# Performance work log

Measured on AMD Instinct MI355X. Metric: run time of the kernel, lower is better.

## Reference

```python
import jax, jax.numpy as jnp
import numpy as np


def setup_inputs() -> dict:
    key = jax.random.key(0)
    ks = jax.random.split(key, 16)
    B, S, D, H = 32, 2048, 512, 512
    s = 1.0 / np.sqrt(H)
    inp = {
        "x": jax.random.normal(ks[0], (B, H), jnp.float32),
        "context": jax.random.normal(ks[1], (B, S, D), jnp.float32),
        "mask": jnp.zeros((B, S), jnp.bool_),  # False = valid position
        "Wi": jax.random.normal(ks[2], (H, H), jnp.float32) * s,
        "bi": jax.random.normal(ks[3], (H,), jnp.float32) * s,
        "Wc0": jax.random.normal(ks[4], (H, D), jnp.float32) * s,
        "bc0": jax.random.normal(ks[5], (H,), jnp.float32) * s,
        "Wc1": jax.random.normal(ks[6], (H, D), jnp.float32) * s,
        "bc1": jax.random.normal(ks[7], (H,), jnp.float32) * s,
        "Wc2": jax.random.normal(ks[8], (H, D), jnp.float32) * s,
        "bc2": jax.random.normal(ks[9], (H,), jnp.float32) * s,
        "Wc3": jax.random.normal(ks[10], (H, D), jnp.float32) * s,
        "bc3": jax.random.normal(ks[11], (H,), jnp.float32) * s,
        "V": jax.random.uniform(ks[12], (H,), jnp.float32, -s, s),
    }
    return inp


def reference(x, context, mask, Wi, bi, Wc0, bc0, Wc1, bc1, Wc2, bc2, Wc3, bc3, V):
    # mask: True = masked out in the original API; module flips it first.
    valid = ~mask  # [B, S], True = keep

    inp = (x @ Wi.T + bi)[:, :, None]  # [B, H, 1]

    def proj(W, b):
        # Conv1d(D, H, kernel=1) on context.permute(0,2,1) == token-wise GEMM
        return jnp.einsum("bsd,hd->bhs", context, W) + b[None, :, None]  # [B, H, S]

    ctx = jnp.concatenate(
        [proj(Wc0, bc0), proj(Wc1, bc1), proj(Wc2, bc2), proj(Wc3, bc3)], axis=2
    )  # [B, H, 4S]

    t = jnp.tanh(inp + ctx)                      # [B, H, 4S]
    att = jnp.einsum("h,bhs->bs", V, t)          # bmm(V[B,1,H], t).squeeze(1)
    att = 10.0 * jnp.tanh(att)                   # [B, 4S]

    valid4 = jnp.tile(valid, (1, 4))             # mask.repeat(1, 4)
    att = jnp.where(valid4, att, -jnp.inf)
    # torch.no_grad() around the masked fill detaches the rest of the graph
    att = jax.lax.stop_gradient(att)

    ans = jax.nn.softmax(att, axis=1)            # [B, 4S]
    p = jnp.max(ans, axis=1)
    indices = jnp.argmax(ans, axis=1)
    return indices[:, None], p[:, None], mask
```

## Files before the change

kernel.cpp:

```cpp
#include <hip/hip_runtime.h>
#include <math.h>

typedef __bf16 bf16x8 __attribute__((ext_vector_type(8)));
typedef float f32x4 __attribute__((ext_vector_type(4)));
typedef short short8v __attribute__((ext_vector_type(8)));

#define MARGIN 0.01f
#define NCAND 32

__device__ __forceinline__ unsigned short f2bf(float f) {
  unsigned u = __float_as_uint(f);
  u += 0x7fffu + ((u >> 16) & 1u);
  return (unsigned short)(u >> 16);
}
__device__ __forceinline__ float tanh_fast(float x) {
  float e = __builtin_amdgcn_exp2f(x * 2.885390081777927f);
  return 1.f - 2.f * __builtin_amdgcn_rcpf(e + 1.f);
}
__device__ __forceinline__ void gl_lds16(const void* g, void* l) {
  __builtin_amdgcn_global_load_lds(
      (const __attribute__((address_space(1))) unsigned int*)g,
      (__attribute__((address_space(3))) unsigned int*)l, 16, 0, 0);
}

__global__ __launch_bounds__(256) void prep_inp_k(const float* __restrict__ x,
    const float* __restrict__ Wi, const float* __restrict__ bi, float* __restrict__ inp) {
  int gid = blockIdx.x * 256 + threadIdx.x;
  int b = gid >> 9, h = gid & 511;
  const float* xr = x + b * 512;
  const float* wr = Wi + h * 512;
  float acc = bi[h];
  #pragma unroll 4
  for (int k = 0; k < 512; k += 4) {
    float4 xv = *(const float4*)(xr + k);
    float4 wv = *(const float4*)(wr + k);
    acc += xv.x * wv.x + xv.y * wv.y + xv.z * wv.z + xv.w * wv.w;
  }
  inp[gid] = acc;
}

__global__ __launch_bounds__(256) void prep_w_pack_k(const float* __restrict__ w0,
    const float* __restrict__ w1, const float* __restrict__ w2, const float* __restrict__ w3,
    short* __restrict__ Whi) {
  int gid = blockIdx.x * 256 + threadIdx.x;
  if (gid >= 131072) return;
  int c = gid & 3, row = (gid >> 2) & 255, TK = gid >> 10;
  int TN = TK >> 4, KS = TK & 15;
  int n = TN * 256 + row;
  int g = n >> 9, h = n & 511;
  const float* w = (g == 0) ? w0 : (g == 1) ? w1 : (g == 2) ? w2 : w3;
  int csrc = c ^ ((row >> 1) & 3);
  const float* src = w + (size_t)h * 512 + KS * 32 + csrc * 8;
  float f[8];
  *(float4*)&f[0] = *(const float4*)(src);
  *(float4*)&f[4] = *(const float4*)(src + 4);
  short8v hv;
  #pragma unroll
  for (int i = 0; i < 8; ++i) hv[i] = (short)f2bf(f[i]);
  *(short8v*)(Whi + (size_t)gid * 8) = hv;
}

__global__ __launch_bounds__(256) void prep_ctx_pack_k(const float* __restrict__ ctx,
    short* __restrict__ Chi) {
  int gid = blockIdx.x * 256 + threadIdx.x;
  int c = gid & 3, row = (gid >> 2) & 255, TK = gid >> 10;
  int TM = TK >> 4, KS = TK & 15;
  size_t m = (size_t)TM * 256 + row;
  int csrc = c ^ ((row >> 1) & 3);
  int k = KS * 32 + csrc * 8;
  float f[8];
  *(float4*)&f[0] = *(const float4*)(ctx + m * 512 + k);
  *(float4*)&f[4] = *(const float4*)(ctx + m * 512 + k + 4);
  short8v hv;
  #pragma unroll
  for (int i = 0; i < 8; ++i) hv[i] = (short)f2bf(f[i]);
  *(short8v*)(Chi + (size_t)gid * 8) = hv;
}

template<bool PRESPLIT>
__global__ __launch_bounds__(512, 2) void gemm_att_k(
    const float* __restrict__ ctx, const short* __restrict__ Chi,
    const short* __restrict__ Whi,
    const float* __restrict__ inp,
    const float* __restrict__ bc0, const float* __restrict__ bc1,
    const float* __restrict__ bc2, const float* __restrict__ bc3,
    const float* __restrict__ V, float* __restrict__ att) {
  __shared__ __align__(16) short smem[2][2][8192];
  __shared__ float sV[256], sPre[256];

  const int t = threadIdx.x;
  int d = blockIdx.x + (blockIdx.y << 3);
  int work = (d & 7) * 256 + (d >> 3);
  int mt = work >> 3, nt = work & 7;
  int b = mt >> 3;
  int g = nt >> 1, h0 = (nt & 1) * 256;

  if (t < 256) {
    const float* bc = (g == 0) ? bc0 : (g == 1) ? bc1 : (g == 2) ? bc2 : bc3;
    sV[t] = V[h0 + t];
    sPre[t] = inp[b * 512 + h0 + t] + bc[h0 + t];
  }

  const int toff = t * 8;
  auto stage = [&](int buf, int ks) {
    short* lb = &smem[buf][0][0];
    if (PRESPLIT) {
      const short* gA = Chi + (((size_t)mt * 16 + ks) << 13) + toff;
      gl_lds16(gA,        lb + toff);
      gl_lds16(gA + 4096, lb + toff + 4096);
    } else {
      int row = t >> 1, half = t & 1;
      const float* src = ctx + ((size_t)mt * 256 + row) * 512 + ks * 32 + half * 16;
      float f0[8], f1[8];
      *(float4*)&f0[0] = *(const float4*)(src);
      *(float4*)&f0[4] = *(const float4*)(src + 4);
      *(float4*)&f1[0] = *(const float4*)(src + 8);
      *(float4*)&f1[4] = *(const float4*)(src + 12);
      short8v h0v, h1v;
      #pragma unroll
      for (int i = 0; i < 8; ++i) { h0v[i] = (short)f2bf(f0[i]); h1v[i] = (short)f2bf(f1[i]); }
      int s = (row >> 1) & 3;
      int p0 = (half * 2) ^ s, p1 = (half * 2 + 1) ^ s;
      *(short8v*)&smem[buf][0][row * 32 + p0 * 8] = h0v;
      *(short8v*)&smem[buf][0][row * 32 + p1 * 8] = h1v;
    }
    const short* gB = Whi + (((size_t)nt * 16 + ks) << 13) + toff;
    gl_lds16(gB,        lb + 8192 + toff);
    gl_lds16(gB + 4096, lb + 8192 + toff + 4096);
  };

  f32x4 acc[8][4];
  #pragma unroll
  for (int i = 0; i < 8; ++i)
    #pragma unroll
    for (int j = 0; j < 4; ++j) acc[i][j] = (f32x4){0.f, 0.f, 0.f, 0.f};

  const int lane = t & 63, wid = t >> 6;
  const int wr = wid >> 2, wc = wid & 3;
  const int fr = lane & 15, fq = lane >> 4;
  const int csw = fq ^ ((fr >> 1) & 3);

  stage(0, 0);
  __syncthreads();

  for (int ks = 0; ks < 16; ++ks) {
    int cur = ks & 1;
    if (ks + 1 < 16) stage(cur ^ 1, ks + 1);

    const short* sa = &smem[cur][0][0];
    bf16x8 ah[8], bh[4];
    #pragma unroll
    for (int mi = 0; mi < 8; ++mi)
      ah[mi] = *(const bf16x8*)(sa + (wr * 128 + mi * 16 + fr) * 32 + csw * 8);
    #pragma unroll
    for (int ni = 0; ni < 4; ++ni)
      bh[ni] = *(const bf16x8*)(sa + 8192 + (wc * 64 + ni * 16 + fr) * 32 + csw * 8);
    #pragma unroll
    for (int mi = 0; mi < 8; ++mi)
      #pragma unroll
      for (int ni = 0; ni < 4; ++ni)
        acc[mi][ni] = __builtin_amdgcn_mfma_f32_16x16x32_bf16(ah[mi], bh[ni], acc[mi][ni], 0, 0, 0);
    __syncthreads();
  }

  float vV[4], vP[4];
  #pragma unroll
  for (int ni = 0; ni < 4; ++ni) {
    int j = wc * 64 + ni * 16 + fr;
    vV[ni] = sV[j];
    vP[ni] = sPre[j];
  }
  size_t abase = (size_t)b * 8192 + (size_t)g * 2048;
  #pragma unroll
  for (int mi = 0; mi < 8; ++mi) {
    #pragma unroll
    for (int r = 0; r < 4; ++r) {
      float sum = 0.f;
      #pragma unroll
      for (int ni = 0; ni < 4; ++ni)
        sum += vV[ni] * tanh_fast(vP[ni] + acc[mi][ni][r]);
      sum += __shfl_xor(sum, 1, 64);
      sum += __shfl_xor(sum, 2, 64);
      sum += __shfl_xor(sum, 4, 64);
      sum += __shfl_xor(sum, 8, 64);
      if (fr == 0) {
        int s = (mt * 256 + wr * 128 + mi * 16 + fq * 4 + r) & 2047;
        atomicAdd(&att[abase + s], sum);
      }
    }
  }
}

__global__ __launch_bounds__(256) void tail_k(const float* __restrict__ att,
    const unsigned char* __restrict__ mask, const float* __restrict__ ctx,
    const float* __restrict__ Wc0, const float* __restrict__ Wc1,
    const float* __restrict__ Wc2, const float* __restrict__ Wc3,
    const float* __restrict__ bc0, const float* __restrict__ bc1,
    const float* __restrict__ bc2, const float* __restrict__ bc3,
    const float* __restrict__ inp, const float* __restrict__ V,
    float* __restrict__ out) {
  int b = blockIdx.x, t = threadIdx.x;
  __shared__ float sred[256];
  __shared__ float sctx[512];
  __shared__ int scnt;
  __shared__ int scand_j[NCAND];
  __shared__ float scand_a[NCAND];
  __shared__ float sexact[NCAND];

  if (t == 0) scnt = 0;
  float bm = -1e30f;
  for (int j = t; j < 8192; j += 256) {
    if (mask[b * 2048 + (j & 2047)]) continue;
    bm = fmaxf(bm, att[(size_t)b * 8192 + j]);
  }
  sred[t] = bm;
  __syncthreads();
  for (int s2 = 128; s2 > 0; s2 >>= 1) {
    if (t < s2) sred[t] = fmaxf(sred[t], sred[t + s2]);
    __syncthreads();
  }
  float mx = sred[0];
  float Lref = 10.f * tanhf(mx);
  __syncthreads();
  float se = 0.f;
  for (int j = t; j < 8192; j += 256) {
    if (mask[b * 2048 + (j & 2047)]) continue;
    float a = att[(size_t)b * 8192 + j];
    se += expf(10.f * tanhf(a) - Lref);
    if (a >= mx - MARGIN) {
      int slot = atomicAdd(&scnt, 1);
      if (slot < NCAND) { scand_j[slot] = j; scand_a[slot] = a; }
    }
  }
  sred[t] = se;
  __syncthreads();
  for (int s2 = 128; s2 > 0; s2 >>= 1) {
    if (t < s2) sred[t] += sred[t + s2];
    __syncthreads();
  }
  float den = sred[0];
  int n = min(scnt, NCAND);
  for (int j = t; j < 2048; j += 256)
    out[64 + b * 2048 + j] = mask[b * 2048 + j] ? 1.0f : 0.0f;
  for (int i = 0; i < n; ++i) {
    int jj = scand_j[i];
    int g = jj >> 11, s = jj & 2047;
    const float* W  = (g == 0) ? Wc0 : (g == 1) ? Wc1 : (g == 2) ? Wc2 : Wc3;
    const float* bc = (g == 0) ? bc0 : (g == 1) ? bc1 : (g == 2) ? bc2 : bc3;
    const float* cr = ctx + ((size_t)b * 2048 + s) * 512;
    __syncthreads();
    sctx[t] = cr[t];
    sctx[t + 256] = cr[t + 256];
    __syncthreads();
    float total = 0.f;
    #pragma unroll
    for (int hh = 0; hh < 2; ++hh) {
      int h = t + hh * 256;
      const float* wr = W + (size_t)h * 512;
      float acc = 0.f;
      #pragma unroll 4
      for (int k = 0; k < 512; k += 4) {
        float4 wv = *(const float4*)(wr + k);
        acc += wv.x * sctx[k] + wv.y * sctx[k + 1] + wv.z * sctx[k + 2] + wv.w * sctx[k + 3];
      }
      total += V[h] * tanhf(inp[b * 512 + h] + bc[h] + acc);
    }
    sred[t] = total;
    __syncthreads();
    for (int s2 = 128; s2 > 0; s2 >>= 1) {
      if (t < s2) sred[t] += sred[t + s2];
      __syncthreads();
    }
    if (t == 0) sexact[i] = sred[0];
  }
  __syncthreads();
  if (t == 0) {
    float d = den, best = -1e30f;
    int bj = 0x7fffffff;
    for (int i = 0; i < n; ++i) {
      float e = sexact[i];
      int j = scand_j[i];
      d += expf(10.f * tanhf(e) - Lref) - expf(10.f * tanhf(scand_a[i]) - Lref);
      if (e > best || (e == best && j < bj)) { best = e; bj = j; }
    }
    out[b] = (float)bj;
    out[32 + b] = expf(10.f * tanhf(best) - Lref) / d;
  }
}

extern "C" void kernel_launch(void* const* d_in, const int* in_sizes, int n_in,
                              void* d_out, int out_size, void* d_ws, size_t ws_size,
                              hipStream_t stream) {
  const float* x    = (const float*)d_in[0];
  const float* ctx  = (const float*)d_in[1];
  const unsigned char* mask = (const unsigned char*)d_in[2];
  const float* Wi   = (const float*)d_in[3];
  const float* bi   = (const float*)d_in[4];
  const float* Wc0  = (const float*)d_in[5];
  const float* bc0  = (const float*)d_in[6];
  const float* Wc1  = (const float*)d_in[7];
  const float* bc1  = (const float*)d_in[8];
  const float* Wc2  = (const float*)d_in[9];
  const float* bc2  = (const float*)d_in[10];
  const float* Wc3  = (const float*)d_in[11];
  const float* bc3  = (const float*)d_in[12];
  const float* V    = (const float*)d_in[13];
  float* out = (float*)d_out;

  float* inp    = (float*)d_ws;
  float* att    = inp + 16384;
  short* Whi    = (short*)(att + 262144);
  short* Chi    = Whi + 1048576;
  size_t need = (size_t)((char*)(Chi + 33554432) - (char*)d_ws);
  bool presplit = ws_size >= need;

  hipMemsetAsync(att, 0, 262144 * sizeof(float), stream);
  prep_inp_k<<<64, 256, 0, stream>>>(x, Wi, bi, inp);
  prep_w_pack_k<<<512, 256, 0, stream>>>(Wc0, Wc1, Wc2, Wc3, Whi);
  if (presplit) {
    prep_ctx_pack_k<<<16384, 256, 0, stream>>>(ctx, Chi);
    gemm_att_k<true><<<dim3(8, 256), 512, 0, stream>>>(ctx, Chi, Whi,
        inp, bc0, bc1, bc2, bc3, V, att);
  } else {
    gemm_att_k<false><<<dim3(8, 256), 512, 0, stream>>>(ctx, nullptr, Whi,
        inp, bc0, bc1, bc2, bc3, V, att);
  }
  tail_k<<<32, 256, 0, stream>>>(att, mask, ctx, Wc0, Wc1, Wc2, Wc3,
      bc0, bc1, bc2, bc3, inp, V, out);
}
```

Before: 320.8 us.

## Use 64-wide K tiles with split-phase MFMA/load interleaving in GEMM

Doubles the K-tile from 32 to 64 so the main loop runs 8 iterations instead of 16. The packed bf16 layout and its XOR swizzle are changed to match. Each tile is split into four MFMA phases, with the A and B prefetches staggered between them. Explicit waitcnt, sched_barrier, s_barrier and setprio control the overlap of loads and matrix math. The aim is fewer barriers per K and better hiding of global-to-LDS latency, at the cost of twice the LDS footprint, which may limit the 2-blocks-per-CU occupancy.

Result: no change. 325.2 us (+1.4%).

```diff
diff --git a/kernel.cpp b/kernel.cpp
--- a/kernel.cpp
+++ b/kernel.cpp
@@ -7,6 +7,22 @@
 
 #define MARGIN 0.01f
 #define NCAND 32
+
+#define WAITL do { asm volatile("s_waitcnt lgkmcnt(0)" ::: "memory"); __builtin_amdgcn_sched_barrier(0); } while (0)
+#define WAITV do { asm volatile("s_waitcnt vmcnt(0)" ::: "memory"); __builtin_amdgcn_sched_barrier(0); } while (0)
+#define RBAR  do { __builtin_amdgcn_sched_barrier(0); __builtin_amdgcn_s_barrier(); } while (0)
+#define BARR  __builtin_amdgcn_s_barrier()
+
+#define MFMA_PHASE(NH, B0, B1) do { \
+    WAITL; \
+    __builtin_amdgcn_s_setprio(1); \
+    _Pragma("unroll") \
+    for (int mi = 0; mi < 8; ++mi) { \
+      acc[mi][2*(NH)]   = __builtin_amdgcn_mfma_f32_16x16x32_bf16(a[mi], (B0), acc[mi][2*(NH)],   0, 0, 0); \
+      acc[mi][2*(NH)+1] = __builtin_amdgcn_mfma_f32_16x16x32_bf16(a[mi], (B1), acc[mi][2*(NH)+1], 0, 0, 0); \
+    } \
+    __builtin_amdgcn_s_setprio(0); \
+  } while (0)
 
 __device__ __forceinline__ unsigned short f2bf(float f) {
   unsigned u = __float_as_uint(f);
@@ -44,16 +60,14 @@
     short* __restrict__ Whi) {
   int gid = blockIdx.x * 256 + threadIdx.x;
   if (gid >= 131072) return;
-  int c = gid & 3, row = (gid >> 2) & 255, TK = gid >> 10;
-  int TN = TK >> 4, KS = TK & 15;
-  int n = TN * 256 + row;
+  int s = gid & 7, r = (gid >> 3) & 255, KT = (gid >> 11) & 7, TN = gid >> 14;
+  int n = TN * 256 + r;
   int g = n >> 9, h = n & 511;
   const float* w = (g == 0) ? w0 : (g == 1) ? w1 : (g == 2) ? w2 : w3;
-  int csrc = c ^ ((row >> 1) & 3);
-  const float* src = w + (size_t)h * 512 + KS * 32 + csrc * 8;
+  int k = KT * 64 + ((s ^ (r & 7)) * 8);
   float f[8];
-  *(float4*)&f[0] = *(const float4*)(src);
-  *(float4*)&f[4] = *(const float4*)(src + 4);
+  *(float4*)&f[0] = *(const float4*)(w + (size_t)h * 512 + k);
+  *(float4*)&f[4] = *(const float4*)(w + (size_t)h * 512 + k + 4);
   short8v hv;
   #pragma unroll
   for (int i = 0; i < 8; ++i) hv[i] = (short)f2bf(f[i]);
@@ -63,11 +77,9 @@
 __global__ __launch_bounds__(256) void prep_ctx_pack_k(const float* __restrict__ ctx,
     short* __restrict__ Chi) {
   int gid = blockIdx.x * 256 + threadIdx.x;
-  int c = gid & 3, row = (gid >> 2) & 255, TK = gid >> 10;
-  int TM = TK >> 4, KS = TK & 15;
-  size_t m = (size_t)TM * 256 + row;
-  int csrc = c ^ ((row >> 1) & 3);
-  int k = KS * 32 + csrc * 8;
+  int s = gid & 7, r = (gid >> 3) & 255, KT = (gid >> 11) & 7, TM = gid >> 14;
+  size_t m = (size_t)TM * 256 + r;
+  int k = KT * 64 + ((s ^ (r & 7)) * 8);
   float f[8];
   *(float4*)&f[0] = *(const float4*)(ctx + m * 512 + k);
   *(float4*)&f[4] = *(const float4*)(ctx + m * 512 + k + 4);
@@ -85,7 +97,7 @@
     const float* __restrict__ bc0, const float* __restrict__ bc1,
     const float* __restrict__ bc2, const float* __restrict__ bc3,
     const float* __restrict__ V, float* __restrict__ att) {
-  __shared__ __align__(16) short smem[2][2][8192];
+  __shared__ __align__(16) short smem[2][2][16384];
   __shared__ float sV[256], sPre[256];
 
   const int t = threadIdx.x;
@@ -102,31 +114,37 @@
   }
 
   const int toff = t * 8;
-  auto stage = [&](int buf, int ks) {
-    short* lb = &smem[buf][0][0];
-    if (PRESPLIT) {
-      const short* gA = Chi + (((size_t)mt * 16 + ks) << 13) + toff;
-      gl_lds16(gA,        lb + toff);
-      gl_lds16(gA + 4096, lb + toff + 4096);
-    } else {
-      int row = t >> 1, half = t & 1;
-      const float* src = ctx + ((size_t)mt * 256 + row) * 512 + ks * 32 + half * 16;
-      float f0[8], f1[8];
-      *(float4*)&f0[0] = *(const float4*)(src);
-      *(float4*)&f0[4] = *(const float4*)(src + 4);
-      *(float4*)&f1[0] = *(const float4*)(src + 8);
-      *(float4*)&f1[4] = *(const float4*)(src + 12);
-      short8v h0v, h1v;
+  auto stageA = [&](int tile) {
+    const short* gA = Chi + ((size_t)(mt * 8 + tile)) * 16384 + toff;
+    short* lA = &smem[tile & 1][0][0];
+    gl_lds16(gA,         lA + toff);
+    gl_lds16(gA + 4096,  lA + toff + 4096);
+    gl_lds16(gA + 8192,  lA + toff + 8192);
+    gl_lds16(gA + 12288, lA + toff + 12288);
+  };
+  auto stageB = [&](int tile) {
+    const short* gB = Whi + ((size_t)(nt * 8 + tile)) * 16384 + toff;
+    short* lB = &smem[tile & 1][1][0];
+    gl_lds16(gB,         lB + toff);
+    gl_lds16(gB + 4096,  lB + toff + 4096);
+    gl_lds16(gB + 8192,  lB + toff + 8192);
+    gl_lds16(gB + 12288, lB + toff + 12288);
+  };
+  auto stageA_reg = [&](int tile) {
+    #pragma unroll
+    for (int pass = 0; pass < 4; ++pass) {
+      int cc = pass * 512 + t;
+      int s = cc & 7, r = cc >> 3;
+      int k = tile * 64 + ((s ^ (r & 7)) * 8);
+      const float* src = ctx + ((size_t)mt * 256 + r) * 512 + k;
+      float f[8];
+      *(float4*)&f[0] = *(const float4*)src;
+      *(float4*)&f[4] = *(const float4*)(src + 4);
+      short8v hv;
       #pragma unroll
-      for (int i = 0; i < 8; ++i) { h0v[i] = (short)f2bf(f0[i]); h1v[i] = (short)f2bf(f1[i]); }
-      int s = (row >> 1) & 3;
-      int p0 = (half * 2) ^ s, p1 = (half * 2 + 1) ^ s;
-      *(short8v*)&smem[buf][0][row * 32 + p0 * 8] = h0v;
-      *(short8v*)&smem[buf][0][row * 32 + p1 * 8] = h1v;
-    }
-    const short* gB = Whi + (((size_t)nt * 16 + ks) << 13) + toff;
-    gl_lds16(gB,        lb + 8192 + toff);
-    gl_lds16(gB + 4096, lb + 8192 + toff + 4096);
+      for (int i = 0; i < 8; ++i) hv[i] = (short)f2bf(f[i]);
+      *(short8v*)(&smem[tile & 1][0][r * 64 + s * 8]) = hv;
+    }
   };
 
   f32x4 acc[8][4];
@@ -138,29 +156,48 @@
   const int lane = t & 63, wid = t >> 6;
   const int wr = wid >> 2, wc = wid & 3;
   const int fr = lane & 15, fq = lane >> 4;
-  const int csw = fq ^ ((fr >> 1) & 3);
-
-  stage(0, 0);
-  __syncthreads();
-
-  for (int ks = 0; ks < 16; ++ks) {
-    int cur = ks & 1;
-    if (ks + 1 < 16) stage(cur ^ 1, ks + 1);
-
-    const short* sa = &smem[cur][0][0];
-    bf16x8 ah[8], bh[4];
-    #pragma unroll
-    for (int mi = 0; mi < 8; ++mi)
-      ah[mi] = *(const bf16x8*)(sa + (wr * 128 + mi * 16 + fr) * 32 + csw * 8);
-    #pragma unroll
-    for (int ni = 0; ni < 4; ++ni)
-      bh[ni] = *(const bf16x8*)(sa + 8192 + (wc * 64 + ni * 16 + fr) * 32 + csw * 8);
-    #pragma unroll
-    for (int mi = 0; mi < 8; ++mi)
-      #pragma unroll
-      for (int ni = 0; ni < 4; ++ni)
-        acc[mi][ni] = __builtin_amdgcn_mfma_f32_16x16x32_bf16(ah[mi], bh[ni], acc[mi][ni], 0, 0, 0);
-    __syncthreads();
+  const int slot = fq ^ (fr & 7);
+  const int aoff = (wr * 128 + fr) * 64 + slot * 8;
+  const int boff = (wc * 64 + fr) * 64 + slot * 8;
+
+  if (PRESPLIT) stageA(0); else stageA_reg(0);
+  stageB(0);
+  WAITV;
+  BARR;
+
+  bf16x8 a[8];
+  for (int tt = 0; tt < 8; ++tt) {
+    short* sa = &smem[tt & 1][0][0];
+    short* sb = &smem[tt & 1][1][0];
+    const int ap1 = aoff ^ 32, bp1 = boff ^ 32;
+    bf16x8 b0, b1;
+    #pragma unroll
+    for (int mi = 0; mi < 8; ++mi) a[mi] = *(const bf16x8*)(sa + aoff + mi * 1024);
+    b0 = *(const bf16x8*)(sb + boff);
+    b1 = *(const bf16x8*)(sb + boff + 1024);
+    if (tt < 7) { if (PRESPLIT) stageA(tt + 1); else stageA_reg(tt + 1); }
+    RBAR;
+    MFMA_PHASE(0, b0, b1);
+    BARR;
+    b0 = *(const bf16x8*)(sb + boff + 2048);
+    b1 = *(const bf16x8*)(sb + boff + 3072);
+    if (tt < 7) stageB(tt + 1);
+    RBAR;
+    MFMA_PHASE(1, b0, b1);
+    BARR;
+    #pragma unroll
+    for (int mi = 0; mi < 8; ++mi) a[mi] = *(const bf16x8*)(sa + ap1 + mi * 1024);
+    b0 = *(const bf16x8*)(sb + bp1);
+    b1 = *(const bf16x8*)(sb + bp1 + 1024);
+    RBAR;
+    MFMA_PHASE(0, b0, b1);
+    BARR;
+    b0 = *(const bf16x8*)(sb + bp1 + 2048);
+    b1 = *(const bf16x8*)(sb + bp1 + 3072);
+    RBAR;
+    MFMA_PHASE(1, b0, b1);
+    WAITV;
+    BARR;
   }
 
   float vV[4], vP[4];
@@ -256,11 +293,11 @@
     #pragma unroll
     for (int hh = 0; hh < 2; ++hh) {
       int h = t + hh * 256;
-      const float* wr = W + (size_t)h * 512;
+      const float* wrp = W + (size_t)h * 512;
       float acc = 0.f;
       #pragma unroll 4
       for (int k = 0; k < 512; k += 4) {
-        float4 wv = *(const float4*)(wr + k);
+        float4 wv = *(const float4*)(wrp + k);
         acc += wv.x * sctx[k] + wv.y * sctx[k + 1] + wv.z * sctx[k + 2] + wv.w * sctx[k + 3];
       }
       total += V[h] * tanhf(inp[b * 512 + h] + bc[h] + acc);
@@ -275,16 +312,16 @@
   }
   __syncthreads();
   if (t == 0) {
-    float d = den, best = -1e30f;
+    float dd = den, best = -1e30f;
     int bj = 0x7fffffff;
     for (int i = 0; i < n; ++i) {
       float e = sexact[i];
       int j = scand_j[i];
-      d += expf(10.f * tanhf(e) - Lref) - expf(10.f * tanhf(scand_a[i]) - Lref);
+      dd += expf(10.f * tanhf(e) - Lref) - expf(10.f * tanhf(scand_a[i]) - Lref);
       if (e > best || (e == best && j < bj)) { best = e; bj = j; }
     }
     out[b] = (float)bj;
-    out[32 + b] = expf(10.f * tanhf(best) - Lref) / d;
+    out[32 + b] = expf(10.f * tanhf(best) - Lref) / dd;
   }
 }
 
```
